# Performance work log

Hardware: AMD Instinct MI355X
Metric: run time of the kernel (lower is better)

The kernel has to match this reference:

```python
import jax, jax.numpy as jnp
import numpy as np

W_WIN, ETA, NSUB, GAP = 5, 0.5, 2, 1e-6

# ---------------- host-side (detached) partition helpers ----------------

def _softmax_np(x):
    e = np.exp(x - x.max())
    return e / e.sum()

def _jsd_np(p, q):
    p = p + 1e-8; p = p / p.sum()
    q = q + 1e-8; q = q / q.sum()
    m = 0.5 * (p + q)
    return float(0.5 * (p * np.log(p / m)).sum() + 0.5 * (q * np.log(q / m)).sum())

def _make_increasing_np(t, gap=GAP):
    t = t.copy()
    for i in range(1, len(t)):
        if t[i] - t[i - 1] < gap:
            t[i] = t[i - 1] + gap
    return t

def _apt_partition(embs, times, w=W_WIN, eta=ETA):
    n = len(times)
    if n < 2 * w:
        return [times[0], times[-1]], [(0, n - 1)]
    bounds = [times[0]]; starts = [0]; j = 0
    while j <= n - 2 * w:
        pl = _softmax_np(embs[j:j + w].mean(0))
        pr = _softmax_np(embs[j + w:j + 2 * w].mean(0))
        if _jsd_np(pl, pr) > eta:
            bounds.append((times[j + w - 1] + times[j + w]) / 2.0)
            starts.append(j + w)
            j += w
        else:
            j += 1
    if times[-1] > bounds[-1]:
        bounds.append(times[-1])
    segs = []
    for i, s in enumerate(starts):
        e = starts[i + 1] - 1 if i + 1 < len(starts) else n - 1
        segs.append((s, e))
    return bounds, segs

def _build_plans(enc_np, ht_np, hl_np, pt_np):
    # mirrors encoded.detach() + .item()/.tolist() in the torch code: the
    # change-point partition and time grids are concrete / non-differentiable
    plans = []
    for b in range(enc_np.shape[0]):
        Lb = int(hl_np[b])
        times = [float(t) for t in ht_np[b, :Lb]]
        bounds, segs = _apt_partition(enc_np[b, :Lb], times)
        seg_plans = []
        for si, (s, e) in enumerate(segs):
            t0 = bounds[si]
            t1 = bounds[si + 1] if si + 1 < len(bounds) else bounds[-1]
            ats = sorted(set([t0, t1] + [t for t in times[s:e + 1] if t0 <= t <= t1]))
            ts = _make_increasing_np(np.asarray(ats, np.float64))
            sel = [int(np.argmin(np.abs(ts - ti))) for ti in times[s:e + 1]]
            seg_plans.append((s, e, (ts[1:] - ts[:-1]).astype(np.float32), sel))
        tail = None
        if float(pt_np[b]) > bounds[-1] + 1e-6:
            s, e = segs[-1]
            ts = _make_increasing_np(np.asarray([bounds[-1], float(pt_np[b])], np.float64))
            tail = (s, e, (ts[1:] - ts[:-1]).astype(np.float32))
        plans.append((seg_plans, tail))
    return plans

# ---------------- differentiable forward ----------------

def _forward(params, plans, u, hi, pos, neg):
    (emb_table, mlp_w1, mlp_b1, mlp_w2, mlp_b2, user_table,
     vf_w1, vf_b1, vf_w2, vf_b2, vf_w3, vf_b3) = params
    B, L = hi.shape
    # Encoder: mlp(emb(ids))
    encoded = jax.nn.relu(emb_table[hi] @ mlp_w1 + mlp_b1) @ mlp_w2 + mlp_b2  # (B,L,d)

    def vf(z, env):  # augmented state [z, env]; env part has zero derivative
        x = jnp.concatenate([z, env])
        h1 = jax.nn.softplus(x @ vf_w1 + vf_b1)
        h2 = jax.nn.softplus(h1 @ vf_w2 + vf_b2)
        return h2 @ vf_w3 + vf_b3

    def integrate(z0, env, dts):  # fixed-step Euler, NSUB substeps per interval
        def step(z, dt):
            for _ in range(NSUB):
                z = z + (dt / NSUB) * vf(z, env)
            return z, z
        _, traj = jax.lax.scan(step, z0, jnp.asarray(dts))
        return jnp.concatenate([z0[None], traj], 0)  # (K, d)

    z_out, tz_out = [], []
    for b in range(B):
        seg_plans, tail = plans[b]
        z = user_table[u[b]]
        tz = []
        for (s, e, dts, sel) in seg_plans:
            env = encoded[b, s:e + 1].mean(0)
            if len(dts) == 0:  # degenerate segment (unreachable with this data)
                tz.extend([z] * (e - s + 1))
                continue
            zt = integrate(z, env, dts)
            tz.extend([zt[i] for i in sel])  # state-at-nearest-grid-time matching
            z = zt[-1]
        if tail is not None:  # evolve up to prediction time t_target
            s, e, dts = tail
            z = integrate(z, encoded[b, s:e + 1].mean(0), dts)[-1]
        z_out.append(z)
        tz_out.append(jnp.stack(tz))
    z_final = jnp.stack(z_out)          # (B,d)
    traj_z = jnp.stack(tz_out)          # (B,L,d) evolved states at interaction times
    traj_t = encoded                    # traj targets = encoded items in order
    s_pos = jnp.sum(z_final * emb_table[pos], -1)
    s_neg = jnp.sum(z_final * emb_table[neg], -1)
    return jnp.concatenate([s_pos[:, None], s_neg[:, None],
                            traj_z.reshape(B, -1), traj_t.reshape(B, -1)], -1)


def setup_inputs():
    key = jax.random.key(0)
    ks = jax.random.split(key, 16)
    n_users, n_items, d, h = 10000, 200000, 128, 512
    B, L = 4, 128
    def xavier(k, shape):
        s = (2.0 / (shape[0] + shape[1])) ** 0.5
        return (jax.random.normal(k, shape) * s).astype(jnp.float32)
    inp = {
        'emb_table': xavier(ks[0], (n_items, d)).at[0].set(0.0),  # padding_idx=0
        'mlp_w1': xavier(ks[1], (d, d)), 'mlp_b1': jnp.zeros((d,), jnp.float32),
        'mlp_w2': xavier(ks[2], (d, d)), 'mlp_b2': jnp.zeros((d,), jnp.float32),
        'user_table': xavier(ks[3], (n_users, d)),
        'vf_w1': xavier(ks[4], (2 * d, h)), 'vf_b1': jnp.zeros((h,), jnp.float32),
        'vf_w2': xavier(ks[5], (h, h)), 'vf_b2': jnp.zeros((h,), jnp.float32),
        'vf_w3': xavier(ks[6], (h, d)), 'vf_b3': jnp.zeros((d,), jnp.float32),
        'u': jax.random.randint(ks[7], (B,), 0, n_users),
        'hi': jax.random.randint(ks[8], (B, L), 1, n_items),
        'ht': jnp.sort(jax.random.uniform(ks[9], (B, L)) * 10.0, axis=1).astype(jnp.float32),
        'hl': jnp.full((B,), L, dtype=jnp.int32),
        'pos': jax.random.randint(ks[10], (B,), 1, n_items),
        'neg': jax.random.randint(ks[11], (B,), 1, n_items),
    }
    inp['pt'] = inp['ht'][:, -1] + 1.0
    return inp


def reference(emb_table, mlp_w1, mlp_b1, mlp_w2, mlp_b2, user_table,
              vf_w1, vf_b1, vf_w2, vf_b2, vf_w3, vf_b3,
              u, hi, ht, hl, pt, pos, neg):
    params = (emb_table, mlp_w1, mlp_b1, mlp_w2, mlp_b2, user_table,
              vf_w1, vf_b1, vf_w2, vf_b2, vf_w3, vf_b3)
    enc_np = np.asarray(jax.nn.relu(emb_table[hi] @ mlp_w1 + mlp_b1) @ mlp_w2 + mlp_b2)
    plans = _build_plans(enc_np, np.asarray(ht), np.asarray(hl), np.asarray(pt))
    return _forward(params, plans, u, hi, pos, neg)
```

## Files before the change

### kernel.cpp

```cpp
#include <hip/hip_runtime.h>
#include <math.h>

#define W_WIN 5
#define NSUB 2
#define MAX_SEG 64
#define MAX_T 256
#define NWGB 8

__device__ __forceinline__ float softplusf(float v) {
    return fmaxf(v, 0.0f) + log1pf(expf(-fabsf(v)));
}

__device__ __forceinline__ float npsum128(float e0, float e1) {
    int lane = threadIdx.x & 63;
    int k = lane & 7;
    float r = __shfl(e0, k, 64);
    #pragma unroll
    for (int m = 1; m < 8; ++m) r += __shfl(e0, k + 8 * m, 64);
    #pragma unroll
    for (int m = 0; m < 8; ++m) r += __shfl(e1, k + 8 * m, 64);
    float r0 = __shfl(r, 0, 64), r1 = __shfl(r, 1, 64), r2 = __shfl(r, 2, 64), r3 = __shfl(r, 3, 64);
    float r4 = __shfl(r, 4, 64), r5 = __shfl(r, 5, 64), r6 = __shfl(r, 6, 64), r7 = __shfl(r, 7, 64);
    return ((r0 + r1) + (r2 + r3)) + ((r4 + r5) + (r6 + r7));
}

__device__ __forceinline__ float wmax128(float e0, float e1) {
    float m = fmaxf(e0, e1);
    #pragma unroll
    for (int s = 1; s < 64; s <<= 1) m = fmaxf(m, __shfl_xor(m, s, 64));
    return m;
}

__global__ void encode_kernel(const float* __restrict__ emb, const int* __restrict__ hi,
                              const float* __restrict__ w1, const float* __restrict__ b1,
                              const float* __restrict__ w2, const float* __restrict__ b2,
                              float* __restrict__ enc, float* __restrict__ out,
                              int B, int L, int D) {
    __shared__ float x[128];
    __shared__ float h[128];
    int row = blockIdx.x;
    int j = threadIdx.x;
    int idx = hi[row];
    x[j] = emb[(size_t)idx * D + j];
    __syncthreads();
    float s = b1[j];
    #pragma unroll 8
    for (int i = 0; i < 128; ++i) s += x[i] * w1[i * 128 + j];
    h[j] = fmaxf(s, 0.0f);
    __syncthreads();
    float o = b2[j];
    #pragma unroll 8
    for (int i = 0; i < 128; ++i) o += h[i] * w2[i * 128 + j];
    enc[(size_t)row * D + j] = o;
    int b = row / L, l = row % L;
    size_t OS = 2 + 2 * (size_t)L * D;
    out[(size_t)b * OS + 2 + (size_t)L * D + (size_t)l * D + j] = o;
}

__global__ __launch_bounds__(64) void jsd_kernel(
        const float* __restrict__ enc_all, const int* __restrict__ hl,
        float* __restrict__ jsdv, int L, int D) {
    const int b = blockIdx.x >> 7;
    const int j = blockIdx.x & 127;
    const int n = hl[b];
    if (n < 2 * W_WIN || j > n - 2 * W_WIN) return;
    const int lane = threadIdx.x;
    const float* r = enc_all + ((size_t)b * L + j) * D;
    float ml0 = ((((r[lane]       + r[128 + lane]) + r[256 + lane]) + r[384 + lane]) + r[512 + lane]) / 5.0f;
    float ml1 = ((((r[64 + lane]  + r[192 + lane]) + r[320 + lane]) + r[448 + lane]) + r[576 + lane]) / 5.0f;
    float mr0 = ((((r[640 + lane] + r[768 + lane]) + r[896 + lane]) + r[1024 + lane]) + r[1152 + lane]) / 5.0f;
    float mr1 = ((((r[704 + lane] + r[832 + lane]) + r[960 + lane]) + r[1088 + lane]) + r[1216 + lane]) / 5.0f;
    float mxl = wmax128(ml0, ml1), mxr = wmax128(mr0, mr1);
    float a0 = expf(ml0 - mxl), a1 = expf(ml1 - mxl);
    float c0 = expf(mr0 - mxr), c1 = expf(mr1 - mxr);
    float sl = npsum128(a0, a1), sr = npsum128(c0, c1);
    float p0 = a0 / sl + 1e-8f, p1 = a1 / sl + 1e-8f;
    float q0 = c0 / sr + 1e-8f, q1 = c1 / sr + 1e-8f;
    float sp = npsum128(p0, p1), sq = npsum128(q0, q1);
    p0 /= sp; p1 /= sp; q0 /= sq; q1 /= sq;
    float mv0 = 0.5f * (p0 + q0), mv1 = 0.5f * (p1 + q1);
    float t10 = p0 * logf(p0 / mv0), t11 = p1 * logf(p1 / mv1);
    float t20 = q0 * logf(q0 / mv0), t21 = q1 * logf(q1 / mv1);
    float s1 = npsum128(t10, t11), s2 = npsum128(t20, t21);
    if (lane == 0) jsdv[b * L + j] = 0.5f * s1 + 0.5f * s2;
}

__global__ __launch_bounds__(64) void plan_kernel(
        const float* __restrict__ enc_all, const float* __restrict__ ht,
        const int* __restrict__ hl, const float* __restrict__ pt,
        const float* __restrict__ jsdv,
        float* __restrict__ envs, float* __restrict__ dt_sched,
        int* __restrict__ envid, int* __restrict__ stateidx,
        int* __restrict__ Tcnt, int B, int L, int D) {
    const int b = blockIdx.x;
    const int lane = threadIdx.x;
    const float* encg = enc_all + (size_t)b * L * D;
    const float* times = ht + (size_t)b * L;

    __shared__ float encs[128 * 128];
    __shared__ double cand[160];
    __shared__ double bounds[40];
    __shared__ int starts[40];
    __shared__ int seg_s[40], seg_e[40];
    __shared__ int m_sh;

    for (int v = lane; v < 128 * 128 / 4; v += 64)
        ((float4*)encs)[v] = ((const float4*)encg)[v];
    int n = hl[b];
    __syncthreads();

    int nb = 1, ns = 1;
    if (lane == 0) { bounds[0] = (double)times[0]; starts[0] = 0; }
    __syncthreads();

    if (n >= 2 * W_WIN) {
        int j = 0;
        while (j <= n - 2 * W_WIN) {
            float jsd = jsdv[b * L + j];
            if (jsd > 0.5f) {
                if (nb < 39 && ns < 39) {
                    if (lane == 0) {
                        bounds[nb] = ((double)times[j + W_WIN - 1] + (double)times[j + W_WIN]) * 0.5;
                        starts[ns] = j + W_WIN;
                    }
                    nb++; ns++;
                }
                j += W_WIN;
            } else {
                j += 1;
            }
        }
    }
    __syncthreads();

    {
        double lastb = bounds[nb - 1];
        if ((double)times[n - 1] > lastb) {
            if (lane == 0) bounds[nb] = (double)times[n - 1];
            nb++;
        }
    }
    if (lane == 0) {
        for (int si = 0; si < ns; ++si) {
            seg_s[si] = starts[si];
            seg_e[si] = (si + 1 < ns) ? (starts[si + 1] - 1) : (n - 1);
        }
    }
    __syncthreads();

    int C = 0;
    for (int si = 0; si < ns; ++si) {
        int s = seg_s[si], e = seg_e[si];
        if (lane == 0) {
            double t0 = bounds[si];
            double t1 = (si + 1 < nb) ? bounds[si + 1] : bounds[nb - 1];
            int m = 0;
            cand[m++] = t0;
            for (int l = s; l <= e; ++l) {
                double tv = (double)times[l];
                if (tv < t0 || tv > t1) continue;
                if (tv != cand[m - 1]) cand[m++] = tv;
            }
            if (t1 > cand[m - 1]) cand[m++] = t1;
            for (int k = 1; k < m; ++k)
                if (cand[k] - cand[k - 1] < 1e-6) cand[k] = cand[k - 1] + 1e-6;
            m_sh = m;
        }
        __syncthreads();
        int m = m_sh;
        int K = m - 1;
        if (C + K > MAX_T) K = MAX_T - C;
        for (int k = lane; k < K; k += 64) {
            dt_sched[b * MAX_T + C + k] = (float)(cand[k + 1] - cand[k]);
            envid[b * MAX_T + C + k] = si;
        }
        for (int l = s + lane; l <= e; l += 64) {
            double tv = (double)times[l];
            int best = 0;
            double bd = fabs(cand[0] - tv);
            for (int k = 1; k < m; ++k) {
                double dk = fabs(cand[k] - tv);
                if (dk < bd) { bd = dk; best = k; }
            }
            stateidx[b * L + l] = C + best;
        }
        __syncthreads();
        C += K;
    }

    if (lane == 0) {
        double ptv = (double)pt[b];
        if (ptv > bounds[nb - 1] + 1e-6 && C < MAX_T) {
            double a0d = bounds[nb - 1], a1d = ptv;
            if (a1d - a0d < 1e-6) a1d = a0d + 1e-6;
            dt_sched[b * MAX_T + C] = (float)(a1d - a0d);
            envid[b * MAX_T + C] = ns - 1;
            C++;
        }
        Tcnt[b] = C;
    }
    for (int si = 0; si < ns; ++si) {
        int s = seg_s[si], e = seg_e[si];
        float s0 = 0.0f, s1 = 0.0f;
        for (int l = s; l <= e; ++l) {
            s0 += encs[l * 128 + lane];
            s1 += encs[l * 128 + lane + 64];
        }
        float inv = 1.0f / (float)(e - s + 1);
        envs[((size_t)b * MAX_SEG + si) * 128 + lane] = s0 * inv;
        envs[((size_t)b * MAX_SEG + si) * 128 + lane + 64] = s1 * inv;
    }
}

typedef unsigned long long u64;
__device__ __forceinline__ void publish(u64* slot, float v, int phase) {
    u64 pk = ((u64)(unsigned)phase << 32) | (u64)__float_as_uint(v);
    __hip_atomic_store(slot, pk, __ATOMIC_RELAXED, __HIP_MEMORY_SCOPE_AGENT);
}
__device__ __forceinline__ float consume(const u64* slot, int phase) {
    for (;;) {
        u64 pk = __hip_atomic_load(slot, __ATOMIC_RELAXED, __HIP_MEMORY_SCOPE_AGENT);
        if ((int)(pk >> 32) == phase) return __uint_as_float((unsigned)pk);
        __builtin_amdgcn_s_sleep(1);
    }
}

__global__ __launch_bounds__(512, 1) void ode_coop(
    const float* __restrict__ usert, const int* __restrict__ u,
    const float* __restrict__ vw1, const float* __restrict__ vb1,
    const float* __restrict__ vw2, const float* __restrict__ vb2,
    const float* __restrict__ vw3, const float* __restrict__ vb3,
    const float* __restrict__ emb, const int* __restrict__ pos, const int* __restrict__ neg,
    const float* __restrict__ envs, const float* __restrict__ dtsch,
    const int* __restrict__ envid, const int* __restrict__ stidx,
    const int* __restrict__ Tc,
    u64* h1st, u64* zpst,
    float* out, int B)
{
    const int batch = blockIdx.x & 7;
    if (batch >= B) return;
    const int g = blockIdx.x >> 3;
    const int tid = threadIdx.x;

    const int cl = tid >> 3, q = tid & 7;
    const int c12 = g * 64 + cl;
    const int cz = tid >> 2, r = tid & 3;

    __shared__ float xs[256];
    __shared__ float h1s[512];
    __shared__ float h2s[64];
    __shared__ int sidx_sh[128];
    __shared__ float dts_sh[MAX_T];
    __shared__ int sid_sh[MAX_T];

    float w1r[32], w2r[64], w3p[16];
    #pragma unroll
    for (int k4 = 0; k4 < 8; ++k4) {
        int jj = ((k4 + q) & 7) * 4;
        #pragma unroll
        for (int m = 0; m < 4; ++m)
            w1r[k4 * 4 + m] = vw1[(size_t)(q * 32 + jj + m) * 512 + c12];
    }
    #pragma unroll
    for (int k4 = 0; k4 < 16; ++k4) {
        int jj = ((k4 + 2 * q) & 15) * 4;
        #pragma unroll
        for (int m = 0; m < 4; ++m)
            w2r[k4 * 4 + m] = vw2[(size_t)(q * 64 + jj + m) * 512 + c12];
    }
    #pragma unroll
    for (int k = 0; k < 16; ++k)
        w3p[k] = vw3[(size_t)(g * 64 + r * 16 + k) * 128 + cz];
    const float bias1 = vb1[c12];
    const float bias2 = vb2[c12];
    const float b3c = (tid < 128) ? vb3[tid] : 0.0f;

    if (tid < 128) sidx_sh[tid] = stidx[batch * 128 + tid];
    if (tid < MAX_T) {
        dts_sh[tid] = dtsch[batch * MAX_T + tid];
        sid_sh[tid] = envid[batch * MAX_T + tid];
    }

    const int T = Tc[batch];
    u64* h1b = h1st + batch * 512;
    u64* zpb = zpst + batch * 1024;
    const size_t OS = 2 + 2 * (size_t)128 * 128;
    float* outb = out + (size_t)batch * OS;

    if (tid < 128) xs[tid] = usert[(size_t)u[batch] * 128 + tid];
    __syncthreads();

    int lp = 0;
    if (g == 0) {
        while (lp < 128 && sidx_sh[lp] == 0) {
            if (tid < 128) outb[2 + (size_t)lp * 128 + tid] = xs[tid];
            ++lp;
        }
    }

    int phase = 0;
    for (int t = 0; t < T; ++t) {
        const int si = sid_sh[t];
        const float hdt = dts_sh[t] * 0.5f;
        const float* envp = envs + ((size_t)batch * MAX_SEG + si) * 128;
        if (tid >= 128 && tid < 256) xs[tid] = envp[tid - 128];
        __syncthreads();
        #pragma unroll
        for (int sub = 0; sub < NSUB; ++sub) {
            ++phase;
            float acc = 0.0f;
            #pragma unroll
            for (int k4 = 0; k4 < 8; ++k4) {
                int off = q * 32 + ((k4 + q) & 7) * 4;
                float4 xv = *(const float4*)(xs + off);
                acc += w1r[k4 * 4 + 0] * xv.x + w1r[k4 * 4 + 1] * xv.y
                     + w1r[k4 * 4 + 2] * xv.z + w1r[k4 * 4 + 3] * xv.w;
            }
            #pragma unroll
            for (int s = 1; s < 8; s <<= 1) acc += __shfl_xor(acc, s, 64);
            if (q == 0) publish(&h1b[c12], softplusf(acc + bias1), phase);
            h1s[tid] = consume(&h1b[tid], phase);
            __syncthreads();
            acc = 0.0f;
            #pragma unroll
            for (int k4 = 0; k4 < 16; ++k4) {
                int off = q * 64 + ((k4 + 2 * q) & 15) * 4;
                float4 xv = *(const float4*)(h1s + off);
                acc += w2r[k4 * 4 + 0] * xv.x + w2r[k4 * 4 + 1] * xv.y
                     + w2r[k4 * 4 + 2] * xv.z + w2r[k4 * 4 + 3] * xv.w;
            }
            #pragma unroll
            for (int s = 1; s < 8; s <<= 1) acc += __shfl_xor(acc, s, 64);
            if (q == 0) h2s[cl] = softplusf(acc + bias2);
            __syncthreads();
            float az = 0.0f;
            #pragma unroll
            for (int k4 = 0; k4 < 4; ++k4) {
                float4 hv = *(const float4*)(h2s + r * 16 + k4 * 4);
                az += w3p[k4 * 4 + 0] * hv.x + w3p[k4 * 4 + 1] * hv.y
                    + w3p[k4 * 4 + 2] * hv.z + w3p[k4 * 4 + 3] * hv.w;
            }
            az += __shfl_xor(az, 1, 64);
            az += __shfl_xor(az, 2, 64);
            if (r == 0) publish(&zpb[g * 128 + cz], az, phase);
            if (tid < 128) {
                u64 pk[8];
                for (;;) {
                    #pragma unroll
                    for (int g2 = 0; g2 < 8; ++g2)
                        pk[g2] = __hip_atomic_load(&zpb[g2 * 128 + tid],
                                                   __ATOMIC_RELAXED, __HIP_MEMORY_SCOPE_AGENT);
                    bool ok = true;
                    #pragma unroll
                    for (int g2 = 0; g2 < 8; ++g2) ok &= ((int)(pk[g2] >> 32) == phase);
                    if (ok) break;
                    __builtin_amdgcn_s_sleep(1);
                }
                float sum = 0.0f;
                #pragma unroll
                for (int g2 = 0; g2 < 8; ++g2) sum += __uint_as_float((unsigned)pk[g2]);
                xs[tid] = xs[tid] + hdt * (sum + b3c);
            }
            __syncthreads();
        }
        if (g == 0) {
            const int m = t + 1;
            while (lp < 128 && sidx_sh[lp] == m) {
                if (tid < 128) outb[2 + (size_t)lp * 128 + tid] = xs[tid];
                ++lp;
            }
        }
    }
    if (g == 0 && tid < 128) {
        int lane = tid & 63;
        const int item = (tid < 64) ? pos[batch] : neg[batch];
        const float* ev = emb + (size_t)item * 128;
        float sacc = xs[lane] * ev[lane] + xs[lane + 64] * ev[lane + 64];
        #pragma unroll
        for (int s = 1; s < 64; s <<= 1) sacc += __shfl_xor(sacc, s, 64);
        if (lane == 0) outb[(tid < 64) ? 0 : 1] = sacc;
    }
}

extern "C" void kernel_launch(void* const* d_in, const int* in_sizes, int n_in,
                              void* d_out, int out_size, void* d_ws, size_t ws_size,
                              hipStream_t stream) {
    const float* emb   = (const float*)d_in[0];
    const float* w1    = (const float*)d_in[1];
    const float* b1    = (const float*)d_in[2];
    const float* w2    = (const float*)d_in[3];
    const float* b2    = (const float*)d_in[4];
    const float* usert = (const float*)d_in[5];
    const float* vw1   = (const float*)d_in[6];
    const float* vb1   = (const float*)d_in[7];
    const float* vw2   = (const float*)d_in[8];
    const float* vb2   = (const float*)d_in[9];
    const float* vw3   = (const float*)d_in[10];
    const float* vb3   = (const float*)d_in[11];
    const int*   u     = (const int*)d_in[12];
    const int*   hi    = (const int*)d_in[13];
    const float* ht    = (const float*)d_in[14];
    const int*   hl    = (const int*)d_in[15];
    const int*   pos   = (const int*)d_in[16];
    const int*   neg   = (const int*)d_in[17];
    const float* pt    = (const float*)d_in[18];

    int D = in_sizes[2];
    int B = in_sizes[12];
    int L = in_sizes[13] / B;

    u64*   h1st     = (u64*)d_ws;
    u64*   zpst     = h1st + 4 * 512;
    float* jsdv     = (float*)(zpst + 4 * 1024);
    float* enc      = jsdv + (size_t)B * L;
    float* envsb    = enc + (size_t)B * L * D;
    float* dt_sched = envsb + (size_t)B * MAX_SEG * D;
    int*   envid    = (int*)(dt_sched + (size_t)B * MAX_T);
    int*   stateidx = envid + (size_t)B * MAX_T;
    int*   Tcnt     = stateidx + (size_t)B * L;

    hipMemsetAsync(h1st, 0, (4 * 512 + 4 * 1024) * sizeof(u64), stream);
    encode_kernel<<<B * L, D, 0, stream>>>(emb, hi, w1, b1, w2, b2, enc, (float*)d_out, B, L, D);
    jsd_kernel<<<B * 128, 64, 0, stream>>>(enc, hl, jsdv, L, D);
    plan_kernel<<<B, 64, 0, stream>>>(enc, ht, hl, pt, jsdv, envsb, dt_sched, envid, stateidx, Tcnt, B, L, D);
    ode_coop<<<8 * NWGB, 512, 0, stream>>>(usert, u, vw1, vb1, vw2, vb2, vw3, vb3, emb, pos, neg,
                                           envsb, dt_sched, envid, stateidx, Tcnt,
                                           h1st, zpst, (float*)d_out, B);
}
```

Measured before the change: 1.282 ms.

## Repartition ODE MLP across workgroups to need one cross-block exchange per substep

```diff
diff --git a/kernel.cpp b/kernel.cpp
--- a/kernel.cpp
+++ b/kernel.cpp
@@ -217,13 +217,6 @@
     u64 pk = ((u64)(unsigned)phase << 32) | (u64)__float_as_uint(v);
     __hip_atomic_store(slot, pk, __ATOMIC_RELAXED, __HIP_MEMORY_SCOPE_AGENT);
 }
-__device__ __forceinline__ float consume(const u64* slot, int phase) {
-    for (;;) {
-        u64 pk = __hip_atomic_load(slot, __ATOMIC_RELAXED, __HIP_MEMORY_SCOPE_AGENT);
-        if ((int)(pk >> 32) == phase) return __uint_as_float((unsigned)pk);
-        __builtin_amdgcn_s_sleep(1);
-    }
-}
 
 __global__ __launch_bounds__(512, 1) void ode_coop(
     const float* __restrict__ usert, const int* __restrict__ u,
@@ -234,7 +227,7 @@
     const float* __restrict__ envs, const float* __restrict__ dtsch,
     const int* __restrict__ envid, const int* __restrict__ stidx,
     const int* __restrict__ Tc,
-    u64* h1st, u64* zpst,
+    u64* pst,
     float* out, int B)
 {
     const int batch = blockIdx.x & 7;
@@ -243,37 +236,33 @@
     const int tid = threadIdx.x;
 
     const int cl = tid >> 3, q = tid & 7;
-    const int c12 = g * 64 + cl;
     const int cz = tid >> 2, r = tid & 3;
 
+    __shared__ float w1t[64 * 260];
     __shared__ float xs[256];
-    __shared__ float h1s[512];
-    __shared__ float h2s[64];
+    __shared__ float h1loc[64];
+    __shared__ float h2s[512];
     __shared__ int sidx_sh[128];
     __shared__ float dts_sh[MAX_T];
     __shared__ int sid_sh[MAX_T];
 
-    float w1r[32], w2r[64], w3p[16];
+    {
+        const int lane = tid & 63;
+        for (int i = tid >> 6; i < 256; i += 8)
+            w1t[lane * 260 + i] = vw1[(size_t)i * 512 + g * 64 + lane];
+    }
+    float w2r[64];
     #pragma unroll
-    for (int k4 = 0; k4 < 8; ++k4) {
-        int jj = ((k4 + q) & 7) * 4;
-        #pragma unroll
-        for (int m = 0; m < 4; ++m)
-            w1r[k4 * 4 + m] = vw1[(size_t)(q * 32 + jj + m) * 512 + c12];
-    }
+    for (int i = 0; i < 64; ++i)
+        w2r[i] = vw2[(size_t)(g * 64 + i) * 512 + tid];
+    float w3p[128];
     #pragma unroll
-    for (int k4 = 0; k4 < 16; ++k4) {
-        int jj = ((k4 + 2 * q) & 15) * 4;
-        #pragma unroll
-        for (int m = 0; m < 4; ++m)
-            w2r[k4 * 4 + m] = vw2[(size_t)(q * 64 + jj + m) * 512 + c12];
-    }
-    #pragma unroll
-    for (int k = 0; k < 16; ++k)
-        w3p[k] = vw3[(size_t)(g * 64 + r * 16 + k) * 128 + cz];
-    const float bias1 = vb1[c12];
-    const float bias2 = vb2[c12];
-    const float b3c = (tid < 128) ? vb3[tid] : 0.0f;
+    for (int k = 0; k < 128; ++k)
+        w3p[k] = vw3[(size_t)(r * 128 + k) * 128 + cz];
+
+    const float b1c = vb1[g * 64 + cl];
+    const float b2c = vb2[tid];
+    const float b3c = vb3[cz];
 
     if (tid < 128) sidx_sh[tid] = stidx[batch * 128 + tid];
     if (tid < MAX_T) {
@@ -282,8 +271,7 @@
     }
 
     const int T = Tc[batch];
-    u64* h1b = h1st + batch * 512;
-    u64* zpb = zpst + batch * 1024;
+    u64* pbase = pst + (size_t)batch * 8192;
     const size_t OS = 2 + 2 * (size_t)128 * 128;
     float* outb = out + (size_t)batch * OS;
 
@@ -308,59 +296,65 @@
         #pragma unroll
         for (int sub = 0; sub < NSUB; ++sub) {
             ++phase;
-            float acc = 0.0f;
+            float a0 = 0.0f, a1 = 0.0f;
             #pragma unroll
-            for (int k4 = 0; k4 < 8; ++k4) {
-                int off = q * 32 + ((k4 + q) & 7) * 4;
-                float4 xv = *(const float4*)(xs + off);
-                acc += w1r[k4 * 4 + 0] * xv.x + w1r[k4 * 4 + 1] * xv.y
-                     + w1r[k4 * 4 + 2] * xv.z + w1r[k4 * 4 + 3] * xv.w;
-            }
+            for (int i4 = 0; i4 < 8; ++i4) {
+                float4 wv = *(const float4*)(w1t + cl * 260 + q * 32 + i4 * 4);
+                float4 xv = *(const float4*)(xs + q * 32 + i4 * 4);
+                float d = wv.x * xv.x + wv.y * xv.y + wv.z * xv.z + wv.w * xv.w;
+                if (i4 & 1) a1 += d; else a0 += d;
+            }
+            float acc = a0 + a1;
             #pragma unroll
             for (int s = 1; s < 8; s <<= 1) acc += __shfl_xor(acc, s, 64);
-            if (q == 0) publish(&h1b[c12], softplusf(acc + bias1), phase);
-            h1s[tid] = consume(&h1b[tid], phase);
+            if (q == 0) h1loc[cl] = softplusf(acc + b1c);
             __syncthreads();
-            acc = 0.0f;
+            float p0 = 0.0f, p1 = 0.0f, p2 = 0.0f, p3 = 0.0f;
             #pragma unroll
-            for (int k4 = 0; k4 < 16; ++k4) {
-                int off = q * 64 + ((k4 + 2 * q) & 15) * 4;
-                float4 xv = *(const float4*)(h1s + off);
-                acc += w2r[k4 * 4 + 0] * xv.x + w2r[k4 * 4 + 1] * xv.y
-                     + w2r[k4 * 4 + 2] * xv.z + w2r[k4 * 4 + 3] * xv.w;
-            }
+            for (int i4 = 0; i4 < 16; ++i4) {
+                float4 hv = *(const float4*)(h1loc + i4 * 4);
+                float d = w2r[i4 * 4 + 0] * hv.x + w2r[i4 * 4 + 1] * hv.y
+                        + w2r[i4 * 4 + 2] * hv.z + w2r[i4 * 4 + 3] * hv.w;
+                switch (i4 & 3) { case 0: p0 += d; break; case 1: p1 += d; break;
+                                  case 2: p2 += d; break; default: p3 += d; }
+            }
+            float pown = (p0 + p1) + (p2 + p3);
+            u64* pbuf = pbase + (size_t)(phase & 1) * 4096;
+            publish(&pbuf[(size_t)g * 512 + tid], pown, phase);
+            u64 got[8];
+            bool ok;
+            do {
+                ok = true;
+                #pragma unroll
+                for (int g2 = 0; g2 < 8; ++g2)
+                    if (g2 != g)
+                        got[g2] = __hip_atomic_load(&pbuf[(size_t)g2 * 512 + tid],
+                                                    __ATOMIC_RELAXED, __HIP_MEMORY_SCOPE_AGENT);
+                #pragma unroll
+                for (int g2 = 0; g2 < 8; ++g2)
+                    if (g2 != g) ok &= ((int)(got[g2] >> 32) == phase);
+                if (!ok) __builtin_amdgcn_s_sleep(1);
+            } while (!ok);
+            float pv[8];
             #pragma unroll
-            for (int s = 1; s < 8; s <<= 1) acc += __shfl_xor(acc, s, 64);
-            if (q == 0) h2s[cl] = softplusf(acc + bias2);
+            for (int g2 = 0; g2 < 8; ++g2)
+                pv[g2] = (g2 == g) ? pown : __uint_as_float((unsigned)got[g2]);
+            float pre = ((pv[0] + pv[1]) + (pv[2] + pv[3])) + ((pv[4] + pv[5]) + (pv[6] + pv[7]));
+            h2s[tid] = softplusf(pre + b2c);
             __syncthreads();
-            float az = 0.0f;
+            float c0 = 0.0f, c1 = 0.0f, c2 = 0.0f, c3 = 0.0f;
             #pragma unroll
-            for (int k4 = 0; k4 < 4; ++k4) {
-                float4 hv = *(const float4*)(h2s + r * 16 + k4 * 4);
-                az += w3p[k4 * 4 + 0] * hv.x + w3p[k4 * 4 + 1] * hv.y
-                    + w3p[k4 * 4 + 2] * hv.z + w3p[k4 * 4 + 3] * hv.w;
-            }
+            for (int k4 = 0; k4 < 32; ++k4) {
+                float4 hv = *(const float4*)(h2s + r * 128 + k4 * 4);
+                float d = w3p[k4 * 4 + 0] * hv.x + w3p[k4 * 4 + 1] * hv.y
+                        + w3p[k4 * 4 + 2] * hv.z + w3p[k4 * 4 + 3] * hv.w;
+                switch (k4 & 3) { case 0: c0 += d; break; case 1: c1 += d; break;
+                                  case 2: c2 += d; break; default: c3 += d; }
+            }
+            float az = (c0 + c1) + (c2 + c3);
             az += __shfl_xor(az, 1, 64);
             az += __shfl_xor(az, 2, 64);
-            if (r == 0) publish(&zpb[g * 128 + cz], az, phase);
-            if (tid < 128) {
-                u64 pk[8];
-                for (;;) {
-                    #pragma unroll
-                    for (int g2 = 0; g2 < 8; ++g2)
-                        pk[g2] = __hip_atomic_load(&zpb[g2 * 128 + tid],
-                                                   __ATOMIC_RELAXED, __HIP_MEMORY_SCOPE_AGENT);
-                    bool ok = true;
-                    #pragma unroll
-                    for (int g2 = 0; g2 < 8; ++g2) ok &= ((int)(pk[g2] >> 32) == phase);
-                    if (ok) break;
-                    __builtin_amdgcn_s_sleep(1);
-                }
-                float sum = 0.0f;
-                #pragma unroll
-                for (int g2 = 0; g2 < 8; ++g2) sum += __uint_as_float((unsigned)pk[g2]);
-                xs[tid] = xs[tid] + hdt * (sum + b3c);
-            }
+            if (r == 0) xs[cz] = xs[cz] + hdt * (az + b3c);
             __syncthreads();
         }
         if (g == 0) {
@@ -409,9 +403,8 @@
     int B = in_sizes[12];
     int L = in_sizes[13] / B;
 
-    u64*   h1st     = (u64*)d_ws;
-    u64*   zpst     = h1st + 4 * 512;
-    float* jsdv     = (float*)(zpst + 4 * 1024);
+    u64*   pst      = (u64*)d_ws;
+    float* jsdv     = (float*)(pst + 8 * 8192);
     float* enc      = jsdv + (size_t)B * L;
     float* envsb    = enc + (size_t)B * L * D;
     float* dt_sched = envsb + (size_t)B * MAX_SEG * D;
@@ -419,11 +412,11 @@
     int*   stateidx = envid + (size_t)B * MAX_T;
     int*   Tcnt     = stateidx + (size_t)B * L;
 
-    hipMemsetAsync(h1st, 0, (4 * 512 + 4 * 1024) * sizeof(u64), stream);
+    hipMemsetAsync(pst, 0, 8 * 8192 * sizeof(u64), stream);
     encode_kernel<<<B * L, D, 0, stream>>>(emb, hi, w1, b1, w2, b2, enc, (float*)d_out, B, L, D);
     jsd_kernel<<<B * 128, 64, 0, stream>>>(enc, hl, jsdv, L, D);
     plan_kernel<<<B, 64, 0, stream>>>(enc, ht, hl, pt, jsdv, envsb, dt_sched, envid, stateidx, Tcnt, B, L, D);
     ode_coop<<<8 * NWGB, 512, 0, stream>>>(usert, u, vw1, vb1, vw2, vb2, vw3, vb3, emb, pos, neg,
                                            envsb, dt_sched, envid, stateidx, Tcnt,
-                                           h1st, zpst, (float*)d_out, B);
-}
+                                           pst, (float*)d_out, B);
+}
```

Measured after the change: 2.222 ms. 1.73x slower.

## Compute layer-1 redundantly per workgroup to drop the cross-workgroup h1 exchange

Applied to the files above, without the earlier changes.

```diff
diff --git a/kernel.cpp b/kernel.cpp
--- a/kernel.cpp
+++ b/kernel.cpp
@@ -213,16 +213,29 @@
 }
 
 typedef unsigned long long u64;
+
 __device__ __forceinline__ void publish(u64* slot, float v, int phase) {
     u64 pk = ((u64)(unsigned)phase << 32) | (u64)__float_as_uint(v);
     __hip_atomic_store(slot, pk, __ATOMIC_RELAXED, __HIP_MEMORY_SCOPE_AGENT);
 }
-__device__ __forceinline__ float consume(const u64* slot, int phase) {
-    for (;;) {
-        u64 pk = __hip_atomic_load(slot, __ATOMIC_RELAXED, __HIP_MEMORY_SCOPE_AGENT);
-        if ((int)(pk >> 32) == phase) return __uint_as_float((unsigned)pk);
-        __builtin_amdgcn_s_sleep(1);
-    }
+__device__ __forceinline__ u64 ld_agent(const u64* p) {
+    return __hip_atomic_load(p, __ATOMIC_RELAXED, __HIP_MEMORY_SCOPE_AGENT);
+}
+__device__ __forceinline__ void ld8_agent(const u64* b, u64* p) {
+    #pragma unroll
+    for (int i = 0; i < 8; ++i) p[i] = ld_agent(b + i * 128);
+}
+__device__ __forceinline__ bool all8p(const u64* p, int phase) {
+    bool ok = true;
+    #pragma unroll
+    for (int i = 0; i < 8; ++i) ok &= ((int)(p[i] >> 32) == phase);
+    return ok;
+}
+__device__ __forceinline__ float fold8(const u64* p) {
+    float s = 0.0f;
+    #pragma unroll
+    for (int i = 0; i < 8; ++i) s += __uint_as_float((unsigned)p[i]);
+    return s;
 }
 
 __global__ __launch_bounds__(512, 1) void ode_coop(
@@ -234,7 +247,7 @@
     const float* __restrict__ envs, const float* __restrict__ dtsch,
     const int* __restrict__ envid, const int* __restrict__ stidx,
     const int* __restrict__ Tc,
-    u64* h1st, u64* zpst,
+    u64* zpst,
     float* out, int B)
 {
     const int batch = blockIdx.x & 7;
@@ -246,6 +259,7 @@
     const int c12 = g * 64 + cl;
     const int cz = tid >> 2, r = tid & 3;
 
+    __shared__ float w2t[64 * 516];
     __shared__ float xs[256];
     __shared__ float h1s[512];
     __shared__ float h2s[64];
@@ -253,26 +267,30 @@
     __shared__ float dts_sh[MAX_T];
     __shared__ int sid_sh[MAX_T];
 
-    float w1r[32], w2r[64], w3p[16];
-    #pragma unroll
-    for (int k4 = 0; k4 < 8; ++k4) {
-        int jj = ((k4 + q) & 7) * 4;
+    float w1z[128];
+    #pragma unroll
+    for (int q2 = 0; q2 < 4; ++q2) {
         #pragma unroll
-        for (int m = 0; m < 4; ++m)
-            w1r[k4 * 4 + m] = vw1[(size_t)(q * 32 + jj + m) * 512 + c12];
-    }
-    #pragma unroll
-    for (int k4 = 0; k4 < 16; ++k4) {
-        int jj = ((k4 + 2 * q) & 15) * 4;
-        #pragma unroll
-        for (int m = 0; m < 4; ++m)
-            w2r[k4 * 4 + m] = vw2[(size_t)(q * 64 + jj + m) * 512 + c12];
-    }
+        for (int k4 = 0; k4 < 8; ++k4) {
+            int roff = q2 * 32 + ((k4 + q2) & 7) * 4;
+            #pragma unroll
+            for (int m = 0; m < 4; ++m)
+                w1z[q2 * 32 + k4 * 4 + m] = vw1[(size_t)(roff + m) * 512 + tid];
+        }
+    }
+    #pragma unroll 4
+    for (int k = 0; k < 64; ++k) {
+        int j = k * 8 + (tid >> 6);
+        int cl2 = tid & 63;
+        w2t[cl2 * 516 + j] = vw2[(size_t)j * 512 + g * 64 + cl2];
+    }
+    float w3p[16];
     #pragma unroll
     for (int k = 0; k < 16; ++k)
         w3p[k] = vw3[(size_t)(g * 64 + r * 16 + k) * 128 + cz];
-    const float bias1 = vb1[c12];
-    const float bias2 = vb2[c12];
+
+    const float bias1v = vb1[tid];
+    const float bias2  = vb2[c12];
     const float b3c = (tid < 128) ? vb3[tid] : 0.0f;
 
     if (tid < 128) sidx_sh[tid] = stidx[batch * 128 + tid];
@@ -282,8 +300,7 @@
     }
 
     const int T = Tc[batch];
-    u64* h1b = h1st + batch * 512;
-    u64* zpb = zpst + batch * 1024;
+    u64* zpb = zpst + (size_t)batch * 2048;
     const size_t OS = 2 + 2 * (size_t)128 * 128;
     float* outb = out + (size_t)batch * OS;
 
@@ -298,40 +315,99 @@
         }
     }
 
+    float c1nb = 0.0f;
+    int prev_si = -1;
     int phase = 0;
     for (int t = 0; t < T; ++t) {
         const int si = sid_sh[t];
         const float hdt = dts_sh[t] * 0.5f;
-        const float* envp = envs + ((size_t)batch * MAX_SEG + si) * 128;
-        if (tid >= 128 && tid < 256) xs[tid] = envp[tid - 128];
-        __syncthreads();
+        if (si != prev_si) {
+            prev_si = si;
+            const float* envp = envs + ((size_t)batch * MAX_SEG + si) * 128;
+            if (tid >= 128 && tid < 256) xs[tid] = envp[tid - 128];
+            __syncthreads();
+            float p4 = 0.0f, p5 = 0.0f, p6 = 0.0f, p7 = 0.0f;
+            #pragma unroll
+            for (int k4 = 0; k4 < 8; ++k4) {
+                {
+                    int roff = 4 * 32 + ((k4 + 4) & 7) * 4;
+                    float4 xv = *(const float4*)(xs + roff);
+                    p4 += vw1[(size_t)(roff + 0) * 512 + tid] * xv.x
+                        + vw1[(size_t)(roff + 1) * 512 + tid] * xv.y
+                        + vw1[(size_t)(roff + 2) * 512 + tid] * xv.z
+                        + vw1[(size_t)(roff + 3) * 512 + tid] * xv.w;
+                }
+                {
+                    int roff = 5 * 32 + ((k4 + 5) & 7) * 4;
+                    float4 xv = *(const float4*)(xs + roff);
+                    p5 += vw1[(size_t)(roff + 0) * 512 + tid] * xv.x
+                        + vw1[(size_t)(roff + 1) * 512 + tid] * xv.y
+                        + vw1[(size_t)(roff + 2) * 512 + tid] * xv.z
+                        + vw1[(size_t)(roff + 3) * 512 + tid] * xv.w;
+                }
+                {
+                    int roff = 6 * 32 + ((k4 + 6) & 7) * 4;
+                    float4 xv = *(const float4*)(xs + roff);
+                    p6 += vw1[(size_t)(roff + 0) * 512 + tid] * xv.x
+                        + vw1[(size_t)(roff + 1) * 512 + tid] * xv.y
+                        + vw1[(size_t)(roff + 2) * 512 + tid] * xv.z
+                        + vw1[(size_t)(roff + 3) * 512 + tid] * xv.w;
+                }
+                {
+                    int roff = 7 * 32 + ((k4 + 7) & 7) * 4;
+                    float4 xv = *(const float4*)(xs + roff);
+                    p7 += vw1[(size_t)(roff + 0) * 512 + tid] * xv.x
+                        + vw1[(size_t)(roff + 1) * 512 + tid] * xv.y
+                        + vw1[(size_t)(roff + 2) * 512 + tid] * xv.z
+                        + vw1[(size_t)(roff + 3) * 512 + tid] * xv.w;
+                }
+            }
+            c1nb = (p4 + p5) + (p6 + p7);
+            __syncthreads();
+        }
         #pragma unroll
         for (int sub = 0; sub < NSUB; ++sub) {
             ++phase;
-            float acc = 0.0f;
-            #pragma unroll
-            for (int k4 = 0; k4 < 8; ++k4) {
-                int off = q * 32 + ((k4 + q) & 7) * 4;
-                float4 xv = *(const float4*)(xs + off);
-                acc += w1r[k4 * 4 + 0] * xv.x + w1r[k4 * 4 + 1] * xv.y
-                     + w1r[k4 * 4 + 2] * xv.z + w1r[k4 * 4 + 3] * xv.w;
-            }
-            #pragma unroll
-            for (int s = 1; s < 8; s <<= 1) acc += __shfl_xor(acc, s, 64);
-            if (q == 0) publish(&h1b[c12], softplusf(acc + bias1), phase);
-            h1s[tid] = consume(&h1b[tid], phase);
+            {
+                float p0 = 0.0f, p1 = 0.0f, p2 = 0.0f, p3 = 0.0f;
+                #pragma unroll
+                for (int k4 = 0; k4 < 8; ++k4) {
+                    {
+                        float4 xv = *(const float4*)(xs + (((k4 + 0) & 7) * 4));
+                        p0 += w1z[k4 * 4 + 0] * xv.x + w1z[k4 * 4 + 1] * xv.y
+                            + w1z[k4 * 4 + 2] * xv.z + w1z[k4 * 4 + 3] * xv.w;
+                    }
+                    {
+                        float4 xv = *(const float4*)(xs + (32 + ((k4 + 1) & 7) * 4));
+                        p1 += w1z[32 + k4 * 4 + 0] * xv.x + w1z[32 + k4 * 4 + 1] * xv.y
+                            + w1z[32 + k4 * 4 + 2] * xv.z + w1z[32 + k4 * 4 + 3] * xv.w;
+                    }
+                    {
+                        float4 xv = *(const float4*)(xs + (64 + ((k4 + 2) & 7) * 4));
+                        p2 += w1z[64 + k4 * 4 + 0] * xv.x + w1z[64 + k4 * 4 + 1] * xv.y
+                            + w1z[64 + k4 * 4 + 2] * xv.z + w1z[64 + k4 * 4 + 3] * xv.w;
+                    }
+                    {
+                        float4 xv = *(const float4*)(xs + (96 + ((k4 + 3) & 7) * 4));
+                        p3 += w1z[96 + k4 * 4 + 0] * xv.x + w1z[96 + k4 * 4 + 1] * xv.y
+                            + w1z[96 + k4 * 4 + 2] * xv.z + w1z[96 + k4 * 4 + 3] * xv.w;
+                    }
+                }
+                float zt = (p0 + p1) + (p2 + p3);
+                h1s[tid] = softplusf((zt + c1nb) + bias1v);
+            }
             __syncthreads();
-            acc = 0.0f;
+            float acc2 = 0.0f;
             #pragma unroll
             for (int k4 = 0; k4 < 16; ++k4) {
-                int off = q * 64 + ((k4 + 2 * q) & 15) * 4;
-                float4 xv = *(const float4*)(h1s + off);
-                acc += w2r[k4 * 4 + 0] * xv.x + w2r[k4 * 4 + 1] * xv.y
-                     + w2r[k4 * 4 + 2] * xv.z + w2r[k4 * 4 + 3] * xv.w;
+                int off = ((k4 + 2 * q) & 15) * 4;
+                float4 wv = *(const float4*)(w2t + cl * 516 + q * 64 + off);
+                float4 hv = *(const float4*)(h1s + q * 64 + off);
+                acc2 += wv.x * hv.x + wv.y * hv.y + wv.z * hv.z + wv.w * hv.w;
             }
             #pragma unroll
-            for (int s = 1; s < 8; s <<= 1) acc += __shfl_xor(acc, s, 64);
-            if (q == 0) h2s[cl] = softplusf(acc + bias2);
+            for (int s = 1; s < 8; s <<= 1) acc2 += __shfl_xor(acc2, s, 64);
+            if (q == 0) h2s[cl] = softplusf(acc2 + bias2);
             __syncthreads();
             float az = 0.0f;
             #pragma unroll
@@ -342,23 +418,16 @@
             }
             az += __shfl_xor(az, 1, 64);
             az += __shfl_xor(az, 2, 64);
-            if (r == 0) publish(&zpb[g * 128 + cz], az, phase);
+            u64* pb = zpb + (size_t)(phase & 1) * 1024;
+            if (r == 0) publish(&pb[g * 128 + cz], az, phase);
             if (tid < 128) {
-                u64 pk[8];
+                u64 s8[8];
                 for (;;) {
-                    #pragma unroll
-                    for (int g2 = 0; g2 < 8; ++g2)
-                        pk[g2] = __hip_atomic_load(&zpb[g2 * 128 + tid],
-                                                   __ATOMIC_RELAXED, __HIP_MEMORY_SCOPE_AGENT);
-                    bool ok = true;
-                    #pragma unroll
-                    for (int g2 = 0; g2 < 8; ++g2) ok &= ((int)(pk[g2] >> 32) == phase);
-                    if (ok) break;
+                    ld8_agent(&pb[tid], s8);
+                    if (all8p(s8, phase)) break;
                     __builtin_amdgcn_s_sleep(1);
                 }
-                float sum = 0.0f;
-                #pragma unroll
-                for (int g2 = 0; g2 < 8; ++g2) sum += __uint_as_float((unsigned)pk[g2]);
+                float sum = fold8(s8);
                 xs[tid] = xs[tid] + hdt * (sum + b3c);
             }
             __syncthreads();
@@ -409,9 +478,8 @@
     int B = in_sizes[12];
     int L = in_sizes[13] / B;
 
-    u64*   h1st     = (u64*)d_ws;
-    u64*   zpst     = h1st + 4 * 512;
-    float* jsdv     = (float*)(zpst + 4 * 1024);
+    u64*   zpst     = (u64*)d_ws;
+    float* jsdv     = (float*)(zpst + 4 * 2048);
     float* enc      = jsdv + (size_t)B * L;
     float* envsb    = enc + (size_t)B * L * D;
     float* dt_sched = envsb + (size_t)B * MAX_SEG * D;
@@ -419,11 +487,11 @@
     int*   stateidx = envid + (size_t)B * MAX_T;
     int*   Tcnt     = stateidx + (size_t)B * L;
 
-    hipMemsetAsync(h1st, 0, (4 * 512 + 4 * 1024) * sizeof(u64), stream);
+    hipMemsetAsync(zpst, 0, 4 * 2048 * sizeof(u64), stream);
     encode_kernel<<<B * L, D, 0, stream>>>(emb, hi, w1, b1, w2, b2, enc, (float*)d_out, B, L, D);
     jsd_kernel<<<B * 128, 64, 0, stream>>>(enc, hl, jsdv, L, D);
     plan_kernel<<<B, 64, 0, stream>>>(enc, ht, hl, pt, jsdv, envsb, dt_sched, envid, stateidx, Tcnt, B, L, D);
     ode_coop<<<8 * NWGB, 512, 0, stream>>>(usert, u, vw1, vb1, vw2, vb2, vw3, vb3, emb, pos, neg,
                                            envsb, dt_sched, envid, stateidx, Tcnt,
-                                           h1st, zpst, (float*)d_out, B);
-}
+                                           zpst, (float*)d_out, B);
+}
```

After: 1.578 ms. +23.0%, slower.
